# Optimization experiments

Hardware: AMD Instinct MI355X
Metric: run time of the kernel (lower is better)

The kernel has to match this reference:

```python
import jax, jax.numpy as jnp
import numpy as np

B, IN, H, NB = 8192, 1024, 2048, 8
BS = H // NB  # 256


def setup_inputs() -> dict:
    key = jax.random.key(0)
    ks = jax.random.split(key, 4)
    s = 0.02
    return {
        "x": jax.random.normal(ks[0], (B, IN), dtype=jnp.float32),
        "h": jax.random.normal(ks[1], (B, H), dtype=jnp.float32),
        "W_ir": jax.random.normal(ks[2], (3 * H, IN), dtype=jnp.float32) * s,
        "b_ir_lin": jnp.zeros((3 * H,), dtype=jnp.float32),
        "b_ir": jnp.zeros((3 * H,), dtype=jnp.float32),
        "W_h": jax.random.normal(ks[3], (NB, 3 * BS, BS), dtype=jnp.float32) * s,
        "b_hr": jnp.zeros((3 * H,), dtype=jnp.float32),
    }


def reference(x, h, W_ir, b_ir_lin, b_ir, W_h, b_hr):
    b = x.shape[0]
    nb, three_bs, bs = W_h.shape
    hdim = nb * bs
    # input projection: w_ir(x) + b_ir  -> [B, 3H], chunked globally into r,z,n
    wx = x @ W_ir.T + b_ir_lin + b_ir
    wxr, wxz, wxn = jnp.split(wx, 3, axis=1)
    wxr = wxr.reshape(b, nb, bs)
    wxz = wxz.reshape(b, nb, bs)
    wxn = wxn.reshape(b, nb, bs)
    # block-diagonal hidden projection: per-block Linear(bs -> 3*bs), no bias
    hb = h.reshape(b, nb, bs)
    # b_hr is sliced in contiguous chunks of 3*bs per block (local r,z,n layout)
    wh = jnp.einsum('bki,koi->bko', hb, W_h) + b_hr.reshape(nb, three_bs)
    whr, whz, whn = jnp.split(wh, 3, axis=2)
    r = jax.nn.sigmoid(wxr + whr)
    z = jax.nn.sigmoid(wxz + whz)
    n = jnp.tanh(wxn + r * whn)
    h_new = (1.0 - z) * hb + z * n
    return h_new.reshape(b, hdim)
```

## Files before the change

kernel.cpp:

```cpp
#include <hip/hip_runtime.h>
#include <cstdint>
#include <cstddef>


typedef __attribute__((ext_vector_type(8))) short bf16x8;
typedef __attribute__((ext_vector_type(4))) float f32x4;

__device__ __forceinline__ unsigned short f2bf(float f) {
    uint32_t u = __float_as_uint(f);
    u += 0x7FFFu + ((u >> 16) & 1u);
    return (unsigned short)(u >> 16);
}
__device__ __forceinline__ float bf2f(unsigned short b) {
    return __uint_as_float(((uint32_t)b) << 16);
}

__device__ __forceinline__ void gload16(const void* g, void* l) {
    __builtin_amdgcn_global_load_lds(
        (const __attribute__((address_space(1))) void*)g,
        (__attribute__((address_space(3))) void*)l,
        16, 0, 0);
}

__device__ __forceinline__ float sigmoidf_(float x) {
    return 1.0f / (1.0f + __expf(-x));
}
__device__ __forceinline__ float tanhf_(float x) {
    float e = __expf(-2.0f * fabsf(x));
    float t = (1.0f - e) / (1.0f + e);
    return copysignf(t, x);
}

__global__ __launch_bounds__(256)
void cast_all(const float* __restrict__ x, const float* __restrict__ wir,
              const float* __restrict__ h, const float* __restrict__ wh,
              unsigned short* __restrict__ xb, unsigned short* __restrict__ wirb,
              unsigned short* __restrict__ hb, unsigned short* __restrict__ whb) {
    const int i = blockIdx.x * 256 + threadIdx.x;
    const float* s; unsigned short* d; int j;
    if (i < 2097152)      { s = x;   d = xb;   j = i; }
    else if (i < 3670016) { s = wir; d = wirb; j = i - 2097152; }
    else if (i < 7864320) { s = h;   d = hb;   j = i - 3670016; }
    else                  { s = wh;  d = whb;  j = i - 7864320; }
    const float4 v = *reinterpret_cast<const float4*>(s + (size_t)j * 4);
    ushort4 o;
    o.x = f2bf(v.x); o.y = f2bf(v.y); o.z = f2bf(v.z); o.w = f2bf(v.w);
    *reinterpret_cast<ushort4*>(d + (size_t)j * 4) = o;
}


#define MM24(AV, BV, NT) do {                                                  \
    _Pragma("unroll")                                                          \
    for (int m_ = 0; m_ < 4; ++m_) {                                           \
        acc[0][m_][0] = __builtin_amdgcn_mfma_f32_16x16x32_bf16(               \
            AV[m_], BV[0][0], acc[0][m_][0], 0, 0, 0);                         \
        acc[0][m_][1] = __builtin_amdgcn_mfma_f32_16x16x32_bf16(               \
            AV[m_], BV[0][1], acc[0][m_][1], 0, 0, 0);                         \
        acc[1][m_][0] = __builtin_amdgcn_mfma_f32_16x16x32_bf16(               \
            AV[m_], BV[1][0], acc[1][m_][0], 0, 0, 0);                         \
        acc[1][m_][1] = __builtin_amdgcn_mfma_f32_16x16x32_bf16(               \
            AV[m_], BV[1][1], acc[1][m_][1], 0, 0, 0);                         \
        acc[NT][m_][0] = __builtin_amdgcn_mfma_f32_16x16x32_bf16(              \
            AV[m_], BV[2][0], acc[NT][m_][0], 0, 0, 0);                        \
        acc[NT][m_][1] = __builtin_amdgcn_mfma_f32_16x16x32_bf16(              \
            AV[m_], BV[2][1], acc[NT][m_][1], 0, 0, 0);                        \
    }                                                                          \
} while (0)

#define RDSET(AV, BV, sl, kbx) do {                                            \
    _Pragma("unroll")                                                          \
    for (int m_ = 0; m_ < 4; ++m_)                                             \
        AV[m_] = *(const bf16x8*)(pAr[sl] + m_ * 1024 + (kbx));                \
    _Pragma("unroll")                                                          \
    for (int s_ = 0; s_ < 3; ++s_) {                                           \
        BV[s_][0] = *(const bf16x8*)(pBr[sl] + s_ * 4096 + (kbx));             \
        BV[s_][1] = *(const bf16x8*)(pBr[sl] + s_ * 4096 + 1024 + (kbx));      \
    }                                                                          \
} while (0)

#define I_1(kt, ds) do {                                                       \
    gload16(XbB  + 0 * 32768   + (kt) * 64, As + (ds) * 8192 + 0 * 2048 + doff); \
    gload16(XbB  + 1 * 32768   + (kt) * 64, As + (ds) * 8192 + 1 * 2048 + doff); \
    gload16(XbB  + 2 * 32768   + (kt) * 64, As + (ds) * 8192 + 2 * 2048 + doff); \
    gload16(XbB  + 3 * 32768   + (kt) * 64, As + (ds) * 8192 + 3 * 2048 + doff); \
    gload16(WirB + 0 * 2097152 + 0 * 32768 + (kt) * 64, Bs + (ds) * 12288 + 0 * 2048 + doff); \
    gload16(WirB + 0 * 2097152 + 1 * 32768 + (kt) * 64, Bs + (ds) * 12288 + 1 * 2048 + doff); \
    gload16(WirB + 1 * 2097152 + 0 * 32768 + (kt) * 64, Bs + (ds) * 12288 + 2 * 2048 + doff); \
    gload16(WirB + 1 * 2097152 + 1 * 32768 + (kt) * 64, Bs + (ds) * 12288 + 3 * 2048 + doff); \
    gload16(WirB + 2 * 2097152 + 0 * 32768 + (kt) * 64, Bs + (ds) * 12288 + 4 * 2048 + doff); \
    gload16(WirB + 2 * 2097152 + 1 * 32768 + (kt) * 64, Bs + (ds) * 12288 + 5 * 2048 + doff); \
} while (0)
#define I_2(k2, ds) do {                                                       \
    gload16(XhB + 0 * 65536 + (k2) * 64, As + (ds) * 8192 + 0 * 2048 + doff);  \
    gload16(XhB + 1 * 65536 + (k2) * 64, As + (ds) * 8192 + 1 * 2048 + doff);  \
    gload16(XhB + 2 * 65536 + (k2) * 64, As + (ds) * 8192 + 2 * 2048 + doff);  \
    gload16(XhB + 3 * 65536 + (k2) * 64, As + (ds) * 8192 + 3 * 2048 + doff);  \
    gload16(WhB + 0 * 65536 + 0 * 8192 + (k2) * 64, Bs + (ds) * 12288 + 0 * 2048 + doff); \
    gload16(WhB + 0 * 65536 + 1 * 8192 + (k2) * 64, Bs + (ds) * 12288 + 1 * 2048 + doff); \
    gload16(WhB + 1 * 65536 + 0 * 8192 + (k2) * 64, Bs + (ds) * 12288 + 2 * 2048 + doff); \
    gload16(WhB + 1 * 65536 + 1 * 8192 + (k2) * 64, Bs + (ds) * 12288 + 3 * 2048 + doff); \
    gload16(WhB + 2 * 65536 + 0 * 8192 + (k2) * 64, Bs + (ds) * 12288 + 4 * 2048 + doff); \
    gload16(WhB + 2 * 65536 + 1 * 8192 + (k2) * 64, Bs + (ds) * 12288 + 5 * 2048 + doff); \
} while (0)

#define BODY(sl, STAGE, NTp, NTc) do {                                         \
    asm volatile("s_waitcnt lgkmcnt(0)" ::: "memory");                         \
    asm volatile("s_waitcnt vmcnt(0)" ::: "memory");                           \
    __builtin_amdgcn_s_barrier();                                              \
    STAGE;                                                                     \
    RDSET(avA, bvA, sl, kb0);                                                  \
    MM24(avB, bvB, NTp);                                                       \
    RDSET(avB, bvB, sl, kb1);                                                  \
    MM24(avA, bvA, NTc);                                                       \
} while (0)

__global__ __launch_bounds__(256, 2)
void gru_fused(const unsigned short* __restrict__ Xb,
               const unsigned short* __restrict__ Wirb,
               const unsigned short* __restrict__ Hbb,
               const unsigned short* __restrict__ Whb,
               const float* __restrict__ b_ir_lin,
               const float* __restrict__ b_ir,
               const float* __restrict__ b_hr,
               float* __restrict__ out) {
    constexpr int K1 = 1024, H = 2048;
    __shared__ unsigned short lds[2 * 8192 + 2 * 12288];
    unsigned short* const As = lds;
    unsigned short* const Bs = lds + 2 * 8192;

    const int tid  = threadIdx.x;
    const int lane = tid & 63;
    const int w    = tid >> 6;
    const int wm   = w >> 1;
    const int wn   = w & 1;

    const int bid  = blockIdx.x;
    const int kb   = bid & 7;
    const int idx  = bid >> 3;
    const int bm   = (idx >> 2) * 128;
    const int hsub = idx & 3;
    const int hcb  = kb * 256 + hsub * 64;

    const int srow  = tid >> 3;
    const int chunk = (tid & 7) ^ (srow & 7);
    const int scol  = chunk * 8;
    const int doff  = tid * 8;
    const unsigned short* XbB  = Xb   + (size_t)(bm + srow) * K1 + scol;
    const unsigned short* WirB = Wirb + (size_t)(hcb + srow) * K1 + scol;
    const unsigned short* XhB  = Hbb  + (size_t)(bm + srow) * H + kb * 256 + scol;
    const unsigned short* WhB  = Whb  + (size_t)kb * 196608
                                      + (size_t)(hsub * 64 + srow) * 256 + scol;

    const int fr  = lane & 15;
    const int k0e = (lane >> 4) * 8;
    const int mfr = (fr & 7) << 4;
    const int kb0 = ((k0e * 2) ^ mfr) >> 1;
    const int kb1 = (((k0e * 2) + 64) ^ mfr) >> 1;
    const unsigned short* pAr[2];
    const unsigned short* pBr[2];
    pAr[0] = As + (wm * 64 + fr) * 64;
    pAr[1] = As + 8192 + (wm * 64 + fr) * 64;
    pBr[0] = Bs + (wn * 32 + fr) * 64;
    pBr[1] = Bs + 12288 + (wn * 32 + fr) * 64;

    f32x4 acc[4][4][2] = {};
    bf16x8 avA[4], avB[4], bvA[3][2], bvB[3][2];

    I_1(0, 0);
    asm volatile("s_waitcnt vmcnt(0)" ::: "memory");
    __builtin_amdgcn_s_barrier();
    I_1(1, 1);
    RDSET(avA, bvA, 0, kb0);
    RDSET(avB, bvB, 0, kb1);
    MM24(avA, bvA, 2);

    BODY(1, I_1(2, 0),  2, 2);
    BODY(0, I_1(3, 1),  2, 2);
    BODY(1, I_1(4, 0),  2, 2);
    BODY(0, I_1(5, 1),  2, 2);
    BODY(1, I_1(6, 0),  2, 2);
    BODY(0, I_1(7, 1),  2, 2);
    BODY(1, I_1(8, 0),  2, 2);
    BODY(0, I_1(9, 1),  2, 2);
    BODY(1, I_1(10, 0), 2, 2);
    BODY(0, I_1(11, 1), 2, 2);
    BODY(1, I_1(12, 0), 2, 2);
    BODY(0, I_1(13, 1), 2, 2);
    BODY(1, I_1(14, 0), 2, 2);
    BODY(0, I_1(15, 1), 2, 2);
    BODY(1, I_2(0, 0),  2, 2);
    BODY(0, I_2(1, 1),  2, 3);
    BODY(1, I_2(2, 0),  3, 3);
    BODY(0, I_2(3, 1),  3, 3);
    BODY(1, ((void)0),  3, 3);
    MM24(avB, bvB, 3);

    const int rq = (lane >> 4) * 4;
    #pragma unroll
    for (int n = 0; n < 2; ++n) {
        const int hcol = hcb + wn * 32 + n * 16 + fr;
        const int lcol = hcol & 255;
        const float bir0 = b_ir_lin[hcol]        + b_ir[hcol];
        const float bir1 = b_ir_lin[2048 + hcol] + b_ir[2048 + hcol];
        const float bir2 = b_ir_lin[4096 + hcol] + b_ir[4096 + hcol];
        const float bhr0 = b_hr[kb * 768 + lcol];
        const float bhr1 = b_hr[kb * 768 + 256 + lcol];
        const float bhr2 = b_hr[kb * 768 + 512 + lcol];
        #pragma unroll
        for (int mi = 0; mi < 4; ++mi) {
            #pragma unroll
            for (int r = 0; r < 4; ++r) {
                const int row = bm + wm * 64 + mi * 16 + rq + r;
                const float pr = acc[0][mi][n][r] + bir0 + bhr0;
                const float pz = acc[1][mi][n][r] + bir1 + bhr1;
                const float xn = acc[2][mi][n][r] + bir2;
                const float hn = acc[3][mi][n][r] + bhr2;
                const float rg = sigmoidf_(pr);
                const float zg = sigmoidf_(pz);
                const float ng = tanhf_(xn + rg * hn);
                const float hv = bf2f(Hbb[(size_t)row * H + hcol]);
                out[(size_t)row * H + hcol] = (1.0f - zg) * hv + zg * ng;
            }
        }
    }
}

extern "C" void kernel_launch(void* const* d_in, const int* in_sizes, int n_in,
                              void* d_out, int out_size, void* d_ws, size_t ws_size,
                              hipStream_t stream) {
    const float* x        = (const float*)d_in[0];
    const float* h        = (const float*)d_in[1];
    const float* W_ir     = (const float*)d_in[2];
    const float* b_ir_lin = (const float*)d_in[3];
    const float* b_ir     = (const float*)d_in[4];
    const float* W_h      = (const float*)d_in[5];
    const float* b_hr     = (const float*)d_in[6];
    float* out = (float*)d_out;

    char* ws = (char*)d_ws;
    unsigned short* xb   = (unsigned short*)(ws);
    unsigned short* wirb = (unsigned short*)(ws + 16777216);
    unsigned short* hb   = (unsigned short*)(ws + 29360128);
    unsigned short* whb  = (unsigned short*)(ws + 62914560);

    cast_all<<<32256, 256, 0, stream>>>(x, W_ir, h, W_h, xb, wirb, hb, whb);

    gru_fused<<<2048, 256, 0, stream>>>(xb, wirb, hb, whb,
                                        b_ir_lin, b_ir, b_hr, out);
}
```

Baseline: 176.9 us.

## Enlarge GRU GEMM tile to 256 rows with 512 threads and triple-buffered A

Doubles the M tile per workgroup to 256 rows using 8 waves (2x4 layout), halving the grid and giving each weight tile more reuse across rows. The A operand moves to a three-stage LDS ring with partial vmcnt waits, so the next loads can stay in flight while the current tile is consumed. Each wave now holds 8 M-fragments by 1 N-fragment, which changes the register and LDS pressure. LDS use grows to about 144KB per block, and the launch bounds of 512 threads with 2 blocks per CU may not both fit.

Measured after the change: 181.1 us. 2.3% more time.

```diff
diff --git a/kernel.cpp b/kernel.cpp
--- a/kernel.cpp
+++ b/kernel.cpp
@@ -49,72 +49,65 @@
 }
 
 
-#define MM24(AV, BV, NT) do {                                                  \
-    _Pragma("unroll")                                                          \
-    for (int m_ = 0; m_ < 4; ++m_) {                                           \
-        acc[0][m_][0] = __builtin_amdgcn_mfma_f32_16x16x32_bf16(               \
-            AV[m_], BV[0][0], acc[0][m_][0], 0, 0, 0);                         \
-        acc[0][m_][1] = __builtin_amdgcn_mfma_f32_16x16x32_bf16(               \
-            AV[m_], BV[0][1], acc[0][m_][1], 0, 0, 0);                         \
-        acc[1][m_][0] = __builtin_amdgcn_mfma_f32_16x16x32_bf16(               \
-            AV[m_], BV[1][0], acc[1][m_][0], 0, 0, 0);                         \
-        acc[1][m_][1] = __builtin_amdgcn_mfma_f32_16x16x32_bf16(               \
-            AV[m_], BV[1][1], acc[1][m_][1], 0, 0, 0);                         \
-        acc[NT][m_][0] = __builtin_amdgcn_mfma_f32_16x16x32_bf16(              \
-            AV[m_], BV[2][0], acc[NT][m_][0], 0, 0, 0);                        \
-        acc[NT][m_][1] = __builtin_amdgcn_mfma_f32_16x16x32_bf16(              \
-            AV[m_], BV[2][1], acc[NT][m_][1], 0, 0, 0);                        \
+#define MM24(KH, NT) do {                                                      \
+    _Pragma("unroll")                                                          \
+    for (int m_ = 0; m_ < 8; ++m_) {                                           \
+        acc[0][m_]  = __builtin_amdgcn_mfma_f32_16x16x32_bf16(                 \
+            av[m_], bv[0][KH], acc[0][m_], 0, 0, 0);                           \
+        acc[1][m_]  = __builtin_amdgcn_mfma_f32_16x16x32_bf16(                 \
+            av[m_], bv[1][KH], acc[1][m_], 0, 0, 0);                           \
+        acc[NT][m_] = __builtin_amdgcn_mfma_f32_16x16x32_bf16(                 \
+            av[m_], bv[2][KH], acc[NT][m_], 0, 0, 0);                          \
     }                                                                          \
 } while (0)
 
-#define RDSET(AV, BV, sl, kbx) do {                                            \
-    _Pragma("unroll")                                                          \
-    for (int m_ = 0; m_ < 4; ++m_)                                             \
-        AV[m_] = *(const bf16x8*)(pAr[sl] + m_ * 1024 + (kbx));                \
+#define SB1(kt, ds) do {                                                       \
+    gload16(WirB + 0 * 2097152 + (kt) * 64, Bs + (ds) * 12288 + 0 * 4096 + doff); \
+    gload16(WirB + 1 * 2097152 + (kt) * 64, Bs + (ds) * 12288 + 1 * 4096 + doff); \
+    gload16(WirB + 2 * 2097152 + (kt) * 64, Bs + (ds) * 12288 + 2 * 4096 + doff); \
+} while (0)
+#define SA1(kt, ds) do {                                                       \
+    gload16(XbB + 0 * 65536 + (kt) * 64, As + (ds) * 16384 + 0 * 4096 + doff); \
+    gload16(XbB + 1 * 65536 + (kt) * 64, As + (ds) * 16384 + 1 * 4096 + doff); \
+    gload16(XbB + 2 * 65536 + (kt) * 64, As + (ds) * 16384 + 2 * 4096 + doff); \
+    gload16(XbB + 3 * 65536 + (kt) * 64, As + (ds) * 16384 + 3 * 4096 + doff); \
+} while (0)
+#define SB2(k2, ds) do {                                                       \
+    gload16(WhB + 0 * 65536 + (k2) * 64, Bs + (ds) * 12288 + 0 * 4096 + doff); \
+    gload16(WhB + 1 * 65536 + (k2) * 64, Bs + (ds) * 12288 + 1 * 4096 + doff); \
+    gload16(WhB + 2 * 65536 + (k2) * 64, Bs + (ds) * 12288 + 2 * 4096 + doff); \
+} while (0)
+#define SA2(k2, ds) do {                                                       \
+    gload16(XhB + 0 * 131072 + (k2) * 64, As + (ds) * 16384 + 0 * 4096 + doff); \
+    gload16(XhB + 1 * 131072 + (k2) * 64, As + (ds) * 16384 + 1 * 4096 + doff); \
+    gload16(XhB + 2 * 131072 + (k2) * 64, As + (ds) * 16384 + 2 * 4096 + doff); \
+    gload16(XhB + 3 * 131072 + (k2) * 64, As + (ds) * 16384 + 3 * 4096 + doff); \
+} while (0)
+#define SNOP ((void)0)
+
+#define KBODY(sa, sb, WT, STB, STA, NT) do {                                   \
+    asm volatile("s_waitcnt vmcnt(" WT ")" ::: "memory");                      \
+    __builtin_amdgcn_s_barrier();                                              \
+    STB;                                                                       \
+    STA;                                                                       \
+    const unsigned short* aS = As + (sa) * 16384;                              \
+    const unsigned short* bS = Bs + (sb) * 12288;                              \
+    _Pragma("unroll")                                                          \
+    for (int m_ = 0; m_ < 8; ++m_)                                             \
+        av[m_] = *(const bf16x8*)(aS + (wm * 128 + m_ * 16 + fr) * 64 + kb0);  \
     _Pragma("unroll")                                                          \
     for (int s_ = 0; s_ < 3; ++s_) {                                           \
-        BV[s_][0] = *(const bf16x8*)(pBr[sl] + s_ * 4096 + (kbx));             \
-        BV[s_][1] = *(const bf16x8*)(pBr[sl] + s_ * 4096 + 1024 + (kbx));      \
+        bv[s_][0] = *(const bf16x8*)(bS + (s_ * 64 + wn * 16 + fr) * 64 + kb0);\
+        bv[s_][1] = *(const bf16x8*)(bS + (s_ * 64 + wn * 16 + fr) * 64 + kb1);\
     }                                                                          \
-} while (0)
-
-#define I_1(kt, ds) do {                                                       \
-    gload16(XbB  + 0 * 32768   + (kt) * 64, As + (ds) * 8192 + 0 * 2048 + doff); \
-    gload16(XbB  + 1 * 32768   + (kt) * 64, As + (ds) * 8192 + 1 * 2048 + doff); \
-    gload16(XbB  + 2 * 32768   + (kt) * 64, As + (ds) * 8192 + 2 * 2048 + doff); \
-    gload16(XbB  + 3 * 32768   + (kt) * 64, As + (ds) * 8192 + 3 * 2048 + doff); \
-    gload16(WirB + 0 * 2097152 + 0 * 32768 + (kt) * 64, Bs + (ds) * 12288 + 0 * 2048 + doff); \
-    gload16(WirB + 0 * 2097152 + 1 * 32768 + (kt) * 64, Bs + (ds) * 12288 + 1 * 2048 + doff); \
-    gload16(WirB + 1 * 2097152 + 0 * 32768 + (kt) * 64, Bs + (ds) * 12288 + 2 * 2048 + doff); \
-    gload16(WirB + 1 * 2097152 + 1 * 32768 + (kt) * 64, Bs + (ds) * 12288 + 3 * 2048 + doff); \
-    gload16(WirB + 2 * 2097152 + 0 * 32768 + (kt) * 64, Bs + (ds) * 12288 + 4 * 2048 + doff); \
-    gload16(WirB + 2 * 2097152 + 1 * 32768 + (kt) * 64, Bs + (ds) * 12288 + 5 * 2048 + doff); \
-} while (0)
-#define I_2(k2, ds) do {                                                       \
-    gload16(XhB + 0 * 65536 + (k2) * 64, As + (ds) * 8192 + 0 * 2048 + doff);  \
-    gload16(XhB + 1 * 65536 + (k2) * 64, As + (ds) * 8192 + 1 * 2048 + doff);  \
-    gload16(XhB + 2 * 65536 + (k2) * 64, As + (ds) * 8192 + 2 * 2048 + doff);  \
-    gload16(XhB + 3 * 65536 + (k2) * 64, As + (ds) * 8192 + 3 * 2048 + doff);  \
-    gload16(WhB + 0 * 65536 + 0 * 8192 + (k2) * 64, Bs + (ds) * 12288 + 0 * 2048 + doff); \
-    gload16(WhB + 0 * 65536 + 1 * 8192 + (k2) * 64, Bs + (ds) * 12288 + 1 * 2048 + doff); \
-    gload16(WhB + 1 * 65536 + 0 * 8192 + (k2) * 64, Bs + (ds) * 12288 + 2 * 2048 + doff); \
-    gload16(WhB + 1 * 65536 + 1 * 8192 + (k2) * 64, Bs + (ds) * 12288 + 3 * 2048 + doff); \
-    gload16(WhB + 2 * 65536 + 0 * 8192 + (k2) * 64, Bs + (ds) * 12288 + 4 * 2048 + doff); \
-    gload16(WhB + 2 * 65536 + 1 * 8192 + (k2) * 64, Bs + (ds) * 12288 + 5 * 2048 + doff); \
-} while (0)
-
-#define BODY(sl, STAGE, NTp, NTc) do {                                         \
-    asm volatile("s_waitcnt lgkmcnt(0)" ::: "memory");                         \
-    asm volatile("s_waitcnt vmcnt(0)" ::: "memory");                           \
-    __builtin_amdgcn_s_barrier();                                              \
-    STAGE;                                                                     \
-    RDSET(avA, bvA, sl, kb0);                                                  \
-    MM24(avB, bvB, NTp);                                                       \
-    RDSET(avB, bvB, sl, kb1);                                                  \
-    MM24(avA, bvA, NTc);                                                       \
-} while (0)
-
-__global__ __launch_bounds__(256, 2)
+    MM24(0, NT);                                                               \
+    _Pragma("unroll")                                                          \
+    for (int m_ = 0; m_ < 8; ++m_)                                             \
+        av[m_] = *(const bf16x8*)(aS + (wm * 128 + m_ * 16 + fr) * 64 + kb1);  \
+    MM24(1, NT);                                                               \
+} while (0)
+
+__global__ __launch_bounds__(512, 2)
 void gru_fused(const unsigned short* __restrict__ Xb,
                const unsigned short* __restrict__ Wirb,
                const unsigned short* __restrict__ Hbb,
@@ -124,20 +117,20 @@
                const float* __restrict__ b_hr,
                float* __restrict__ out) {
     constexpr int K1 = 1024, H = 2048;
-    __shared__ unsigned short lds[2 * 8192 + 2 * 12288];
+    __shared__ unsigned short lds[3 * 16384 + 2 * 12288];
     unsigned short* const As = lds;
-    unsigned short* const Bs = lds + 2 * 8192;
+    unsigned short* const Bs = lds + 3 * 16384;
 
     const int tid  = threadIdx.x;
     const int lane = tid & 63;
     const int w    = tid >> 6;
-    const int wm   = w >> 1;
-    const int wn   = w & 1;
+    const int wm   = w >> 2;
+    const int wn   = w & 3;
 
     const int bid  = blockIdx.x;
     const int kb   = bid & 7;
     const int idx  = bid >> 3;
-    const int bm   = (idx >> 2) * 128;
+    const int bm   = (idx >> 2) * 256;
     const int hsub = idx & 3;
     const int hcb  = kb * 256 + hsub * 64;
 
@@ -156,71 +149,56 @@
     const int mfr = (fr & 7) << 4;
     const int kb0 = ((k0e * 2) ^ mfr) >> 1;
     const int kb1 = (((k0e * 2) + 64) ^ mfr) >> 1;
-    const unsigned short* pAr[2];
-    const unsigned short* pBr[2];
-    pAr[0] = As + (wm * 64 + fr) * 64;
-    pAr[1] = As + 8192 + (wm * 64 + fr) * 64;
-    pBr[0] = Bs + (wn * 32 + fr) * 64;
-    pBr[1] = Bs + 12288 + (wn * 32 + fr) * 64;
-
-    f32x4 acc[4][4][2] = {};
-    bf16x8 avA[4], avB[4], bvA[3][2], bvB[3][2];
-
-    I_1(0, 0);
-    asm volatile("s_waitcnt vmcnt(0)" ::: "memory");
-    __builtin_amdgcn_s_barrier();
-    I_1(1, 1);
-    RDSET(avA, bvA, 0, kb0);
-    RDSET(avB, bvB, 0, kb1);
-    MM24(avA, bvA, 2);
-
-    BODY(1, I_1(2, 0),  2, 2);
-    BODY(0, I_1(3, 1),  2, 2);
-    BODY(1, I_1(4, 0),  2, 2);
-    BODY(0, I_1(5, 1),  2, 2);
-    BODY(1, I_1(6, 0),  2, 2);
-    BODY(0, I_1(7, 1),  2, 2);
-    BODY(1, I_1(8, 0),  2, 2);
-    BODY(0, I_1(9, 1),  2, 2);
-    BODY(1, I_1(10, 0), 2, 2);
-    BODY(0, I_1(11, 1), 2, 2);
-    BODY(1, I_1(12, 0), 2, 2);
-    BODY(0, I_1(13, 1), 2, 2);
-    BODY(1, I_1(14, 0), 2, 2);
-    BODY(0, I_1(15, 1), 2, 2);
-    BODY(1, I_2(0, 0),  2, 2);
-    BODY(0, I_2(1, 1),  2, 3);
-    BODY(1, I_2(2, 0),  3, 3);
-    BODY(0, I_2(3, 1),  3, 3);
-    BODY(1, ((void)0),  3, 3);
-    MM24(avB, bvB, 3);
-
-    const int rq = (lane >> 4) * 4;
+
+    f32x4 acc[4][8] = {};
+    bf16x8 av[8], bv[3][2];
+
+    SB1(0, 0); SA1(0, 0); SA1(1, 1);
+
+    KBODY(0, 0, "4", SB1(1, 1),  SA1(2, 2),  2);
+    KBODY(1, 1, "4", SB1(2, 0),  SA1(3, 0),  2);
+    KBODY(2, 0, "4", SB1(3, 1),  SA1(4, 1),  2);
+    KBODY(0, 1, "4", SB1(4, 0),  SA1(5, 2),  2);
+    KBODY(1, 0, "4", SB1(5, 1),  SA1(6, 0),  2);
+    KBODY(2, 1, "4", SB1(6, 0),  SA1(7, 1),  2);
+    KBODY(0, 0, "4", SB1(7, 1),  SA1(8, 2),  2);
+    KBODY(1, 1, "4", SB1(8, 0),  SA1(9, 0),  2);
+    KBODY(2, 0, "4", SB1(9, 1),  SA1(10, 1), 2);
+    KBODY(0, 1, "4", SB1(10, 0), SA1(11, 2), 2);
+    KBODY(1, 0, "4", SB1(11, 1), SA1(12, 0), 2);
+    KBODY(2, 1, "4", SB1(12, 0), SA1(13, 1), 2);
+    KBODY(0, 0, "4", SB1(13, 1), SA1(14, 2), 2);
+    KBODY(1, 1, "4", SB1(14, 0), SA1(15, 0), 2);
+    KBODY(2, 0, "4", SB1(15, 1), SA2(0, 1),  2);
+    KBODY(0, 1, "4", SB2(0, 0),  SA2(1, 2),  2);
+    KBODY(1, 0, "4", SB2(1, 1),  SA2(2, 0),  3);
+    KBODY(2, 1, "4", SB2(2, 0),  SA2(3, 1),  3);
+    KBODY(0, 0, "4", SB2(3, 1),  SNOP,       3);
+    KBODY(1, 1, "0", SNOP,       SNOP,       3);
+
+    const int rq   = (lane >> 4) * 4;
+    const int hcol = hcb + wn * 16 + fr;
+    const int lcol = hcol & 255;
+    const float bir0 = b_ir_lin[hcol]        + b_ir[hcol];
+    const float bir1 = b_ir_lin[2048 + hcol] + b_ir[2048 + hcol];
+    const float bir2 = b_ir_lin[4096 + hcol] + b_ir[4096 + hcol];
+    const float bhr0 = b_hr[kb * 768 + lcol];
+    const float bhr1 = b_hr[kb * 768 + 256 + lcol];
+    const float bhr2 = b_hr[kb * 768 + 512 + lcol];
     #pragma unroll
-    for (int n = 0; n < 2; ++n) {
-        const int hcol = hcb + wn * 32 + n * 16 + fr;
-        const int lcol = hcol & 255;
-        const float bir0 = b_ir_lin[hcol]        + b_ir[hcol];
-        const float bir1 = b_ir_lin[2048 + hcol] + b_ir[2048 + hcol];
-        const float bir2 = b_ir_lin[4096 + hcol] + b_ir[4096 + hcol];
-        const float bhr0 = b_hr[kb * 768 + lcol];
-        const float bhr1 = b_hr[kb * 768 + 256 + lcol];
-        const float bhr2 = b_hr[kb * 768 + 512 + lcol];
+    for (int mi = 0; mi < 8; ++mi) {
         #pragma unroll
-        for (int mi = 0; mi < 4; ++mi) {
-            #pragma unroll
-            for (int r = 0; r < 4; ++r) {
-                const int row = bm + wm * 64 + mi * 16 + rq + r;
-                const float pr = acc[0][mi][n][r] + bir0 + bhr0;
-                const float pz = acc[1][mi][n][r] + bir1 + bhr1;
-                const float xn = acc[2][mi][n][r] + bir2;
-                const float hn = acc[3][mi][n][r] + bhr2;
-                const float rg = sigmoidf_(pr);
-                const float zg = sigmoidf_(pz);
-                const float ng = tanhf_(xn + rg * hn);
-                const float hv = bf2f(Hbb[(size_t)row * H + hcol]);
-                out[(size_t)row * H + hcol] = (1.0f - zg) * hv + zg * ng;
-            }
+        for (int r = 0; r < 4; ++r) {
+            const int row = bm + wm * 128 + mi * 16 + rq + r;
+            const float pr = acc[0][mi][r] + bir0 + bhr0;
+            const float pz = acc[1][mi][r] + bir1 + bhr1;
+            const float xn = acc[2][mi][r] + bir2;
+            const float hn = acc[3][mi][r] + bhr2;
+            const float rg = sigmoidf_(pr);
+            const float zg = sigmoidf_(pz);
+            const float ng = tanhf_(xn + rg * hn);
+            const float hv = bf2f(Hbb[(size_t)row * H + hcol]);
+            out[(size_t)row * H + hcol] = (1.0f - zg) * hv + zg * ng;
         }
     }
 }
@@ -245,6 +223,6 @@
 
     cast_all<<<32256, 256, 0, stream>>>(x, W_ir, h, W_h, xb, wirb, hb, whb);
 
-    gru_fused<<<2048, 256, 0, stream>>>(xb, wirb, hb, whb,
+    gru_fused<<<1024, 512, 0, stream>>>(xb, wirb, hb, whb,
                                         b_ir_lin, b_ir, b_hr, out);
 }
```
